# Kernel optimization log

Measured on AMD Instinct MI355X. Metric: run time of the kernel, lower is better.

Reference implementation:

```python
import jax, jax.numpy as jnp
import numpy as np

B, IN, H1, H2, OUT = 65536, 256, 64, 64, 64
T, ET, ES = 2, 4, 4  # tasks, experts-per-task, shared experts


def _mlp(X, W1, b1, W2, b2, W3, b3):
    # X: [B, IN]; W1: [..., IN, H1] with leading expert dims; returns [B, ..., OUT]
    h = jax.nn.relu(jnp.einsum('bi,...ih->b...h', X, W1) + b1)
    h = jax.nn.relu(jnp.einsum('b...h,...hk->b...k', h, W2) + b2)
    return jnp.einsum('b...k,...ko->b...o', h, W3) + b3


def setup_inputs() -> dict:
    key = jax.random.key(0)
    ks = jax.random.split(key, 16)

    def w(k, shape, fan_in):
        return jax.random.normal(k, shape, dtype=jnp.float32) * (1.0 / np.sqrt(fan_in))

    X = jax.random.normal(ks[0], (B, IN), dtype=jnp.float32)
    # task expert MLPs, batched over [T, ET]
    Wt1 = w(ks[1], (T, ET, IN, H1), IN); bt1 = jnp.zeros((T, ET, H1), jnp.float32)
    Wt2 = w(ks[2], (T, ET, H1, H2), H1); bt2 = jnp.zeros((T, ET, H2), jnp.float32)
    Wt3 = w(ks[3], (T, ET, H2, OUT), H2); bt3 = jnp.zeros((T, ET, OUT), jnp.float32)
    # shared expert MLPs, batched over [ES]
    Ws1 = w(ks[4], (ES, IN, H1), IN); bs1 = jnp.zeros((ES, H1), jnp.float32)
    Ws2 = w(ks[5], (ES, H1, H2), H1); bs2 = jnp.zeros((ES, H2), jnp.float32)
    Ws3 = w(ks[6], (ES, H2, OUT), H2); bs3 = jnp.zeros((ES, OUT), jnp.float32)
    # per-task gates: input -> (ET + ES) logits
    Wg = w(ks[7], (T, IN, ET + ES), IN); bg = jnp.zeros((T, ET + ES), jnp.float32)
    return {"X": X, "Wt1": Wt1, "bt1": bt1, "Wt2": Wt2, "bt2": bt2,
            "Wt3": Wt3, "bt3": bt3, "Ws1": Ws1, "bs1": bs1, "Ws2": Ws2,
            "bs2": bs2, "Ws3": Ws3, "bs3": bs3, "Wg": Wg, "bg": bg}


def reference(X, Wt1, bt1, Wt2, bt2, Wt3, bt3,
              Ws1, bs1, Ws2, bs2, Ws3, bs3, Wg, bg):
    # task experts: [B, T, ET, OUT]; shared experts: [B, ES, OUT]
    task_out = _mlp(X, Wt1, bt1, Wt2, bt2, Wt3, bt3)
    share_out = _mlp(X, Ws1, bs1, Ws2, bs2, Ws3, bs3)
    # concat task + shared experts along the expert axis per task -> [B, T, ET+ES, OUT]
    share_b = jnp.broadcast_to(share_out[:, None], (X.shape[0], T, ES, OUT))
    all_experts = jnp.concatenate([task_out, share_b], axis=2)
    # gates: softmax over experts -> [B, T, ET+ES]
    gates = jax.nn.softmax(jnp.einsum('bi,tie->bte', X, Wg) + bg, axis=-1)
    # gated combine (stack+bmm+squeeze in the original) -> [B, T, OUT]
    return jnp.einsum('bte,bteo->bto', gates, all_experts)
```

## Files before the change

### kernel.cpp

```cpp
#include <hip/hip_runtime.h>
#include <hip/hip_fp16.h>


#define B_TOT   65536
#define IN_DIM  256
#define HD      64
#define NE      12
#define U_A2 49152
#define U_A3 61440
#define U_AG 73728
#define FRAG_BYTES (75776*16)

typedef _Float16 half8  __attribute__((ext_vector_type(8)));
typedef float    f32x16 __attribute__((ext_vector_type(16)));
typedef float    f32x4  __attribute__((ext_vector_type(4)));
typedef unsigned u32x4  __attribute__((ext_vector_type(4)));

__device__ __forceinline__ unsigned short f2h(float x){
  return __builtin_bit_cast(unsigned short, (_Float16)x);
}
__device__ __forceinline__ float h2f(unsigned short u){
  return (float)__builtin_bit_cast(_Float16, u);
}
__device__ __forceinline__ void split2(float x, unsigned short& h, unsigned short& l){
  h = f2h(x); l = f2h(x - h2f(h));
}
__device__ __forceinline__ half8 FRG(u32x4 u){ return __builtin_bit_cast(half8, u); }
__device__ __forceinline__ f32x16 MF(half8 a, half8 b, f32x16 c){
  return __builtin_amdgcn_mfma_f32_32x32x16_f16(a, b, c, 0, 0, 0);
}
__device__ __forceinline__ f32x16 Z16(){
  f32x16 z;
#pragma unroll
  for (int i=0;i<16;i++) z[i]=0.f;
  return z;
}
__device__ __forceinline__ u32x4 lds16(const short* base, int row, int kb){
  return *(const u32x4*)((const char*)base + row*512 + (kb ^ ((row&7)<<4)));
}

__global__ __launch_bounds__(256) void prep(
    const float* __restrict__ Wt1, const float* __restrict__ Ws1,
    const float* __restrict__ Wt2, const float* __restrict__ Ws2,
    const float* __restrict__ Wt3, const float* __restrict__ Ws3,
    const float* __restrict__ Wg,  u32x4* __restrict__ fr){
  int id = blockIdx.x*256 + threadIdx.x;
  if (id >= 37888) return;
  int lane = id & 63;
  int kq   = lane >> 5;
  int row  = lane & 31;
  float v[8];
  unsigned ubase;
  if (id < 24576){
    int r = id >> 6; int kt = r & 15; int rt = (r>>4)&1; int e = r>>5;
    const float* W = (e<8) ? (Wt1 + (size_t)e*(IN_DIM*HD))
                           : (Ws1 + (size_t)(e-8)*(IN_DIM*HD));
    int h = rt*32 + row;
#pragma unroll
    for (int j=0;j<8;j++){ int k = kt*16 + kq*8 + j; v[j] = W[k*HD + h]; }
    ubase = (unsigned)(e*4096 + ((rt*16+kt)*2)*64 + lane);
  } else if (id < 30720){
    int r = (id-24576) >> 6; int kt = r & 3; int rt = (r>>2)&1; int e = r>>3;
    const float* W = (e<8) ? (Wt2 + (size_t)e*(HD*HD))
                           : (Ws2 + (size_t)(e-8)*(HD*HD));
    int h = rt*32 + row;
#pragma unroll
    for (int j=0;j<8;j++){ int k = kt*16 + kq*8 + j; v[j] = W[k*HD + h]; }
    ubase = (unsigned)(U_A2 + e*1024 + ((rt*4+kt)*2)*64 + lane);
  } else if (id < 36864){
    int r = (id-30720) >> 6; int kt = r & 3; int rt = (r>>2)&1; int e = r>>3;
    const float* W = (e<8) ? (Wt3 + (size_t)e*(HD*HD))
                           : (Ws3 + (size_t)(e-8)*(HD*HD));
    int h = rt*32 + row;
#pragma unroll
    for (int j=0;j<8;j++){ int k = kt*16 + kq*8 + j; v[j] = W[k*HD + h]; }
    ubase = (unsigned)(U_A3 + e*1024 + ((rt*4+kt)*2)*64 + lane);
  } else {
    int r = (id-36864) >> 6; int kt = r;
    int g = row;
#pragma unroll
    for (int j=0;j<8;j++){
      int k = kt*16 + kq*8 + j;
      v[j] = (g < 16) ? Wg[(size_t)(g>>3)*(IN_DIM*8) + k*8 + (g&7)] : 0.f;
    }
    ubase = (unsigned)(U_AG + (kt*2)*64 + lane);
  }
  u32x4 uh, ul;
#pragma unroll
  for (int p=0;p<4;p++){
    unsigned short h0,l0,h1,l1;
    split2(v[2*p],h0,l0); split2(v[2*p+1],h1,l1);
    uh[p] = (unsigned)h0 | ((unsigned)h1<<16);
    ul[p] = (unsigned)l0 | ((unsigned)l1<<16);
  }
  fr[ubase]     = uh;
  fr[ubase+64]  = ul;
}

__device__ __forceinline__ void epi12(const f32x16& A, const float* bp, int rt, int hi,
                                      unsigned* oh, unsigned* ol){
#pragma unroll
  for (int p=0;p<8;p++){
    const int j0=2*p, j1=2*p+1;
    float v0 = A[j0] + bp[rt*32 + 8*(j0>>2) + 4*hi + (j0&3)];
    float v1 = A[j1] + bp[rt*32 + 8*(j1>>2) + 4*hi + (j1&3)];
    v0 = fmaxf(v0, 0.f); v1 = fmaxf(v1, 0.f);
    unsigned short h0,l0,h1,l1;
    split2(v0,h0,l0); split2(v1,h1,l1);
    oh[p] = (unsigned)h0 | ((unsigned)h1<<16);
    ol[p] = (unsigned)l0 | ((unsigned)l1<<16);
  }
}

__device__ __forceinline__ half8 bfrag(const unsigned* pk, int kl, int hi){
  unsigned p0 = pk[4*kl+0], p1 = pk[4*kl+1], p2 = pk[4*kl+2], p3 = pk[4*kl+3];
  unsigned q0 = (unsigned)__shfl_xor((int)p0, 32, 64);
  unsigned q1 = (unsigned)__shfl_xor((int)p1, 32, 64);
  unsigned q2 = (unsigned)__shfl_xor((int)p2, 32, 64);
  unsigned q3 = (unsigned)__shfl_xor((int)p3, 32, 64);
  u32x4 u;
  u.x = hi ? q2 : p0;
  u.y = hi ? q3 : p1;
  u.z = hi ? p2 : q0;
  u.w = hi ? p3 : q1;
  return FRG(u);
}

__device__ __forceinline__ void epi3(const f32x16& A, const float* bp, int rt, int ct,
                                     int hi, int li, int e, int lrow0, char* obase){
  unsigned f[8];
#pragma unroll
  for (int p=0;p<8;p++){
    const int j0=2*p, j1=2*p+1;
    float v0 = A[j0] + bp[rt*32 + 8*(j0>>2) + 4*hi + (j0&3)];
    float v1 = A[j1] + bp[rt*32 + 8*(j1>>2) + 4*hi + (j1&3)];
    f[p] = (unsigned)f2h(v0) | ((unsigned)f2h(v1)<<16);
  }
  unsigned g[8];
#pragma unroll
  for (int p=0;p<8;p++) g[p] = (unsigned)__shfl_xor((int)f[p], 32, 64);
  char* ob = obase + ((size_t)(lrow0 + ct*32 + li)*NE + e)*128 + rt*64;
#pragma unroll
  for (int q=0;q<4;q++){
    u32x4 w;
    w.x = hi ? g[2*q]   : f[2*q];
    w.y = hi ? g[2*q+1] : f[2*q+1];
    w.z = hi ? f[2*q]   : g[2*q];
    w.w = hi ? f[2*q+1] : g[2*q+1];
    if ((q>>1) == hi) *(u32x4*)(ob + q*16) = w;
  }
}

#define MM3(ACC, AH, AL, BH, BL) do { \
    ACC = MF(AH,BH,ACC); ACC = MF(AH,BL,ACC); ACC = MF(AL,BH,ACC); } while(0)

__global__ __launch_bounds__(256,2) void moe(
    const float* __restrict__ X,
    const float* __restrict__ bt1, const float* __restrict__ bs1,
    const float* __restrict__ bt2, const float* __restrict__ bs2,
    const float* __restrict__ bt3, const float* __restrict__ bs3,
    const float* __restrict__ bg,  const u32x4* __restrict__ fr,
    float* __restrict__ gout, char* __restrict__ oout, int crow0){
  __shared__ __align__(16) short Xh[64*256];
  __shared__ __align__(16) short Xl[64*256];
  const int t = threadIdx.x;
  const int lrow0 = blockIdx.x*64;
  const int grow0 = crow0 + lrow0;

  {
    const int r = t>>2, cq = t&3;
    const float* xp = X + (size_t)(grow0 + r)*IN_DIM + cq*64;
#pragma unroll
    for (int gq=0; gq<8; gq++){
      f32x4 v0 = *(const f32x4*)(xp + gq*8);
      f32x4 v1 = *(const f32x4*)(xp + gq*8 + 4);
      float vv[8] = {v0.x,v0.y,v0.z,v0.w, v1.x,v1.y,v1.z,v1.w};
      u32x4 uh, ul;
#pragma unroll
      for (int p=0;p<4;p++){
        unsigned short h0,l0,h1,l1;
        split2(vv[2*p],h0,l0); split2(vv[2*p+1],h1,l1);
        uh[p] = (unsigned)h0 | ((unsigned)h1<<16);
        ul[p] = (unsigned)l0 | ((unsigned)l1<<16);
      }
      int kb = (cq*64 + gq*8)*2;
      int addr = r*512 + (kb ^ ((r&7)<<4));
      *(u32x4*)((char*)Xh + addr) = uh;
      *(u32x4*)((char*)Xl + addr) = ul;
    }
  }
  __syncthreads();

  const int wave = t>>6, lane = t&63, li = lane&31, hi = lane>>5;

  if (wave == 0){
    f32x16 g0 = Z16(), g1 = Z16();
    const u32x4* AG = fr + U_AG + lane;
#pragma unroll
    for (int kt=0; kt<16; ++kt){
      half8 ah = FRG(AG[(kt*2+0)*64]);
      half8 al = FRG(AG[(kt*2+1)*64]);
      int kb = kt*32 + hi*16;
      half8 xh0 = FRG(lds16(Xh, li,    kb)), xl0 = FRG(lds16(Xl, li,    kb));
      half8 xh1 = FRG(lds16(Xh, li+32, kb)), xl1 = FRG(lds16(Xl, li+32, kb));
      MM3(g0, ah, al, xh0, xl0);
      MM3(g1, ah, al, xh1, xl1);
    }
#pragma unroll
    for (int ct=0; ct<2; ++ct){
      const f32x16& G = ct ? g1 : g0;
      float own[8], par[8];
#pragma unroll
      for (int j=0;j<8;j++) own[j] = G[j] + bg[8*(j>>2) + 4*hi + (j&3)];
#pragma unroll
      for (int j=0;j<8;j++) par[j] = __shfl_xor(own[j], 32, 64);
      float m0 = fmaxf(fmaxf(fmaxf(own[0],own[1]),fmaxf(own[2],own[3])),
                       fmaxf(fmaxf(par[0],par[1]),fmaxf(par[2],par[3])));
      float m1 = fmaxf(fmaxf(fmaxf(own[4],own[5]),fmaxf(own[6],own[7])),
                       fmaxf(fmaxf(par[4],par[5]),fmaxf(par[6],par[7])));
      float eo[8], ep[8];
#pragma unroll
      for (int j=0;j<4;j++){ eo[j]   = __expf(own[j]-m0);   ep[j]   = __expf(par[j]-m0); }
#pragma unroll
      for (int j=4;j<8;j++){ eo[j]   = __expf(own[j]-m1);   ep[j]   = __expf(par[j]-m1); }
      float s0 = eo[0]+eo[1]+eo[2]+eo[3]+ep[0]+ep[1]+ep[2]+ep[3];
      float s1 = eo[4]+eo[5]+eo[6]+eo[7]+ep[4]+ep[5]+ep[6]+ep[7];
      float i0 = 1.f/s0, i1 = 1.f/s1;
      if (hi == 0){
        float* gp = gout + (size_t)(lrow0 + ct*32 + li)*16;
        f32x4 w;
        w.x=eo[0]*i0; w.y=eo[1]*i0; w.z=eo[2]*i0; w.w=eo[3]*i0; ((f32x4*)gp)[0]=w;
        w.x=ep[0]*i0; w.y=ep[1]*i0; w.z=ep[2]*i0; w.w=ep[3]*i0; ((f32x4*)gp)[1]=w;
        w.x=eo[4]*i1; w.y=eo[5]*i1; w.z=eo[6]*i1; w.w=eo[7]*i1; ((f32x4*)gp)[2]=w;
        w.x=ep[4]*i1; w.y=ep[5]*i1; w.z=ep[6]*i1; w.w=ep[7]*i1; ((f32x4*)gp)[3]=w;
      }
    }
  }

  unsigned opkh[2][2][8], opkl[2][2][8];
#pragma unroll 1
  for (int ei=0; ei<3; ++ei){
    const int e = wave*3 + ei;
    f32x16 a00=Z16(), a01=Z16(), a10=Z16(), a11=Z16();
    const u32x4* A1 = fr + e*4096 + lane;
#pragma unroll
    for (int kt=0; kt<16; ++kt){
      half8 ah0 = FRG(A1[( kt     *2+0)*64]);
      half8 al0 = FRG(A1[( kt     *2+1)*64]);
      half8 ah1 = FRG(A1[((16+kt) *2+0)*64]);
      half8 al1 = FRG(A1[((16+kt) *2+1)*64]);
      int kb = kt*32 + hi*16;
      half8 xh0 = FRG(lds16(Xh, li,    kb)), xl0 = FRG(lds16(Xl, li,    kb));
      half8 xh1 = FRG(lds16(Xh, li+32, kb)), xl1 = FRG(lds16(Xl, li+32, kb));
      MM3(a00, ah0, al0, xh0, xl0);
      MM3(a01, ah0, al0, xh1, xl1);
      MM3(a10, ah1, al1, xh0, xl0);
      MM3(a11, ah1, al1, xh1, xl1);
    }
    const float* b1 = (e<8)? bt1+e*64 : bs1+(e-8)*64;
    epi12(a00,b1,0,hi,opkh[0][0],opkl[0][0]);
    epi12(a01,b1,0,hi,opkh[0][1],opkl[0][1]);
    epi12(a10,b1,1,hi,opkh[1][0],opkl[1][0]);
    epi12(a11,b1,1,hi,opkh[1][1],opkl[1][1]);
    f32x16 c00=Z16(), c01=Z16(), c10=Z16(), c11=Z16();
    const u32x4* A2 = fr + U_A2 + e*1024 + lane;
#pragma unroll
    for (int kt=0; kt<4; ++kt){
      half8 ah0 = FRG(A2[( kt    *2+0)*64]);
      half8 al0 = FRG(A2[( kt    *2+1)*64]);
      half8 ah1 = FRG(A2[((4+kt) *2+0)*64]);
      half8 al1 = FRG(A2[((4+kt) *2+1)*64]);
      const int rs = kt>>1, kl = kt&1;
      half8 bh0 = bfrag(opkh[rs][0], kl, hi), bl0 = bfrag(opkl[rs][0], kl, hi);
      half8 bh1 = bfrag(opkh[rs][1], kl, hi), bl1 = bfrag(opkl[rs][1], kl, hi);
      MM3(c00, ah0, al0, bh0, bl0);
      MM3(c01, ah0, al0, bh1, bl1);
      MM3(c10, ah1, al1, bh0, bl0);
      MM3(c11, ah1, al1, bh1, bl1);
    }
    const float* b2 = (e<8)? bt2+e*64 : bs2+(e-8)*64;
    epi12(c00,b2,0,hi,opkh[0][0],opkl[0][0]);
    epi12(c01,b2,0,hi,opkh[0][1],opkl[0][1]);
    epi12(c10,b2,1,hi,opkh[1][0],opkl[1][0]);
    epi12(c11,b2,1,hi,opkh[1][1],opkl[1][1]);
    f32x16 d00=Z16(), d01=Z16(), d10=Z16(), d11=Z16();
    const u32x4* A3 = fr + U_A3 + e*1024 + lane;
#pragma unroll
    for (int kt=0; kt<4; ++kt){
      half8 ah0 = FRG(A3[( kt    *2+0)*64]);
      half8 al0 = FRG(A3[( kt    *2+1)*64]);
      half8 ah1 = FRG(A3[((4+kt) *2+0)*64]);
      half8 al1 = FRG(A3[((4+kt) *2+1)*64]);
      const int rs = kt>>1, kl = kt&1;
      half8 bh0 = bfrag(opkh[rs][0], kl, hi), bl0 = bfrag(opkl[rs][0], kl, hi);
      half8 bh1 = bfrag(opkh[rs][1], kl, hi), bl1 = bfrag(opkl[rs][1], kl, hi);
      MM3(d00, ah0, al0, bh0, bl0);
      MM3(d01, ah0, al0, bh1, bl1);
      MM3(d10, ah1, al1, bh0, bl0);
      MM3(d11, ah1, al1, bh1, bl1);
    }
    const float* b3 = (e<8)? bt3+e*64 : bs3+(e-8)*64;
    epi3(d00,b3,0,0,hi,li,e,lrow0,oout);
    epi3(d01,b3,0,1,hi,li,e,lrow0,oout);
    epi3(d10,b3,1,0,hi,li,e,lrow0,oout);
    epi3(d11,b3,1,1,hi,li,e,lrow0,oout);
  }
}

__device__ __forceinline__ float2 uph(unsigned u){
  __half2 h = __builtin_bit_cast(__half2, u);
  return __half22float2(h);
}
__global__ __launch_bounds__(256) void comb(
    const u32x4* __restrict__ o, const float* __restrict__ g,
    float* __restrict__ out, int rows, int crow0){
  int tid = blockIdx.x*256 + threadIdx.x;
  if (tid >= rows*4) return;
  int bl = tid>>2, quad = tid&3;
  const u32x4* ob = o + (size_t)bl*96 + quad*2;
  const f32x4* gp = (const f32x4*)(g + (size_t)bl*16);
  f32x4 G0=gp[0], G1=gp[1], G2=gp[2], G3=gp[3];
  float gt[16] = {G0.x,G0.y,G0.z,G0.w, G1.x,G1.y,G1.z,G1.w,
                  G2.x,G2.y,G2.z,G2.w, G3.x,G3.y,G3.z,G3.w};
  float s0[16], s1[16];
#pragma unroll
  for (int i=0;i<16;i++){ s0[i]=0.f; s1[i]=0.f; }
#pragma unroll
  for (int e=0;e<12;e++){
    u32x4 u0 = ob[e*8], u1 = ob[e*8+1];
    float w0 = (e<4) ? gt[e]   : ((e>=8) ? gt[e-4] : 0.f);
    float w1 = (e>=4 && e<8) ? gt[e+4] : ((e>=8) ? gt[e+4] : 0.f);
    float v[16];
#pragma unroll
    for (int p=0;p<4;p++){
      float2 f0 = uph(u0[p]); v[2*p]   = f0.x; v[2*p+1]   = f0.y;
      float2 f1 = uph(u1[p]); v[8+2*p] = f1.x; v[8+2*p+1] = f1.y;
    }
#pragma unroll
    for (int i=0;i<16;i++){ s0[i] += w0*v[i]; s1[i] += w1*v[i]; }
  }
  size_t b = (size_t)crow0 + bl;
  float* op = out + b*128 + quad*16;
#pragma unroll
  for (int p=0;p<4;p++){
    f32x4 w; w.x=s0[4*p]; w.y=s0[4*p+1]; w.z=s0[4*p+2]; w.w=s0[4*p+3];
    *(f32x4*)(op + 4*p) = w;
  }
#pragma unroll
  for (int p=0;p<4;p++){
    f32x4 w; w.x=s1[4*p]; w.y=s1[4*p+1]; w.z=s1[4*p+2]; w.w=s1[4*p+3];
    *(f32x4*)(op + 64 + 4*p) = w;
  }
}

extern "C" void kernel_launch(void* const* d_in, const int* in_sizes, int n_in,
                              void* d_out, int out_size, void* d_ws, size_t ws_size,
                              hipStream_t stream){
  const float* X   = (const float*)d_in[0];
  const float* Wt1 = (const float*)d_in[1];
  const float* bt1 = (const float*)d_in[2];
  const float* Wt2 = (const float*)d_in[3];
  const float* bt2 = (const float*)d_in[4];
  const float* Wt3 = (const float*)d_in[5];
  const float* bt3 = (const float*)d_in[6];
  const float* Ws1 = (const float*)d_in[7];
  const float* bs1 = (const float*)d_in[8];
  const float* Ws2 = (const float*)d_in[9];
  const float* bs2 = (const float*)d_in[10];
  const float* Ws3 = (const float*)d_in[11];
  const float* bs3 = (const float*)d_in[12];
  const float* Wg  = (const float*)d_in[13];
  const float* bg  = (const float*)d_in[14];

  char*  ws = (char*)d_ws;
  u32x4* fr = (u32x4*)ws;
  size_t avail = ws_size > (size_t)FRAG_BYTES ? ws_size - FRAG_BYTES : 0;
  int chunk = B_TOT;
  while (chunk > 64 && (size_t)chunk*1600 > avail) chunk >>= 1;

  hipLaunchKernelGGL(prep, dim3(148), dim3(256), 0, stream,
                     Wt1, Ws1, Wt2, Ws2, Wt3, Ws3, Wg, fr);
  for (int r0 = 0; r0 < B_TOT; r0 += chunk){
    float* gts = (float*)(ws + FRAG_BYTES);
    char*  ob  = ws + FRAG_BYTES + (size_t)chunk*64;
    hipLaunchKernelGGL(moe, dim3(chunk/64), dim3(256), 0, stream,
                       X, bt1, bs1, bt2, bs2, bt3, bs3, bg, fr, gts, ob, r0);
    hipLaunchKernelGGL(comb, dim3((chunk*4+255)/256), dim3(256), 0, stream,
                       (const u32x4*)ob, gts, (float*)d_out, chunk, r0);
  }
}
```

Before: 381.8 us.

## Split MoE kernel into per-expert single-wave blocks with pre-split X in global

X is now converted to fp16 hi/lo pairs once by a separate xsplit kernel that writes to global memory, replacing the per-block LDS staging. The fused moe kernel becomes moe1, which runs one 64-thread wave per (expert, row-group) pair, with an extra block type for the gate softmax. This is meant to raise parallelism and occupancy and to drop the LDS footprint and the block-wide barrier. Layers 2 and 3 are now processed per column tile to lower register pressure, and the expert-output scratch layout is changed to expert-major, with comb re-indexed to match. The cost is extra global traffic for the split X, since every expert block re-reads the hi/lo data from global or L2.

```diff
diff --git a/kernel.cpp b/kernel.cpp
--- a/kernel.cpp
+++ b/kernel.cpp
@@ -15,6 +15,7 @@
 typedef float    f32x16 __attribute__((ext_vector_type(16)));
 typedef float    f32x4  __attribute__((ext_vector_type(4)));
 typedef unsigned u32x4  __attribute__((ext_vector_type(4)));
+typedef unsigned u32x2  __attribute__((ext_vector_type(2)));
 
 __device__ __forceinline__ unsigned short f2h(float x){
   return __builtin_bit_cast(unsigned short, (_Float16)x);
@@ -34,9 +35,6 @@
 #pragma unroll
   for (int i=0;i<16;i++) z[i]=0.f;
   return z;
-}
-__device__ __forceinline__ u32x4 lds16(const short* base, int row, int kb){
-  return *(const u32x4*)((const char*)base + row*512 + (kb ^ ((row&7)<<4)));
 }
 
 __global__ __launch_bounds__(256) void prep(
@@ -97,6 +95,25 @@
   fr[ubase+64]  = ul;
 }
 
+__global__ __launch_bounds__(256) void xsplit(
+    const float* __restrict__ X, u32x2* __restrict__ xh,
+    u32x2* __restrict__ xl, int n4){
+  int tid = blockIdx.x*256 + threadIdx.x;
+  if (tid >= n4) return;
+  f32x4 v = ((const f32x4*)X)[tid];
+  float vv[4] = {v.x, v.y, v.z, v.w};
+  u32x2 uh, ul;
+#pragma unroll
+  for (int p=0;p<2;p++){
+    unsigned short h0,l0,h1,l1;
+    split2(vv[2*p],h0,l0); split2(vv[2*p+1],h1,l1);
+    uh[p] = (unsigned)h0 | ((unsigned)h1<<16);
+    ul[p] = (unsigned)l0 | ((unsigned)l1<<16);
+  }
+  xh[tid] = uh;
+  xl[tid] = ul;
+}
+
 __device__ __forceinline__ void epi12(const f32x16& A, const float* bp, int rt, int hi,
                                       unsigned* oh, unsigned* ol){
 #pragma unroll
@@ -127,7 +144,7 @@
 }
 
 __device__ __forceinline__ void epi3(const f32x16& A, const float* bp, int rt, int ct,
-                                     int hi, int li, int e, int lrow0, char* obase){
+                                     int hi, int li, size_t ebase, char* osc){
   unsigned f[8];
 #pragma unroll
   for (int p=0;p<8;p++){
@@ -139,7 +156,7 @@
   unsigned g[8];
 #pragma unroll
   for (int p=0;p<8;p++) g[p] = (unsigned)__shfl_xor((int)f[p], 32, 64);
-  char* ob = obase + ((size_t)(lrow0 + ct*32 + li)*NE + e)*128 + rt*64;
+  char* ob = osc + (ebase + (size_t)(ct*32 + li))*128 + rt*64;
 #pragma unroll
   for (int q=0;q<4;q++){
     u32x4 w;
@@ -154,64 +171,42 @@
 #define MM3(ACC, AH, AL, BH, BL) do { \
     ACC = MF(AH,BH,ACC); ACC = MF(AH,BL,ACC); ACC = MF(AL,BH,ACC); } while(0)
 
-__global__ __launch_bounds__(256,2) void moe(
-    const float* __restrict__ X,
+__global__ __launch_bounds__(64,3) void moe1(
+    const char* __restrict__ xh, const char* __restrict__ xl,
     const float* __restrict__ bt1, const float* __restrict__ bs1,
     const float* __restrict__ bt2, const float* __restrict__ bs2,
     const float* __restrict__ bt3, const float* __restrict__ bs3,
     const float* __restrict__ bg,  const u32x4* __restrict__ fr,
-    float* __restrict__ gout, char* __restrict__ oout, int crow0){
-  __shared__ __align__(16) short Xh[64*256];
-  __shared__ __align__(16) short Xl[64*256];
-  const int t = threadIdx.x;
-  const int lrow0 = blockIdx.x*64;
-  const int grow0 = crow0 + lrow0;
-
-  {
-    const int r = t>>2, cq = t&3;
-    const float* xp = X + (size_t)(grow0 + r)*IN_DIM + cq*64;
-#pragma unroll
-    for (int gq=0; gq<8; gq++){
-      f32x4 v0 = *(const f32x4*)(xp + gq*8);
-      f32x4 v1 = *(const f32x4*)(xp + gq*8 + 4);
-      float vv[8] = {v0.x,v0.y,v0.z,v0.w, v1.x,v1.y,v1.z,v1.w};
-      u32x4 uh, ul;
-#pragma unroll
-      for (int p=0;p<4;p++){
-        unsigned short h0,l0,h1,l1;
-        split2(vv[2*p],h0,l0); split2(vv[2*p+1],h1,l1);
-        uh[p] = (unsigned)h0 | ((unsigned)h1<<16);
-        ul[p] = (unsigned)l0 | ((unsigned)l1<<16);
-      }
-      int kb = (cq*64 + gq*8)*2;
-      int addr = r*512 + (kb ^ ((r&7)<<4));
-      *(u32x4*)((char*)Xh + addr) = uh;
-      *(u32x4*)((char*)Xl + addr) = ul;
-    }
-  }
-  __syncthreads();
-
-  const int wave = t>>6, lane = t&63, li = lane&31, hi = lane>>5;
-
-  if (wave == 0){
+    float* __restrict__ gout, char* __restrict__ osc, int G, int Crows){
+  const int e = blockIdx.x / G;
+  const int g = blockIdx.x - e*G;
+  const int lane = threadIdx.x, li = lane&31, hi = lane>>5;
+
+  const char* xh0p = xh + (size_t)(g*64 +      li)*512 + hi*16;
+  const char* xh1p = xh + (size_t)(g*64 + 32 + li)*512 + hi*16;
+  const char* xl0p = xl + (size_t)(g*64 +      li)*512 + hi*16;
+  const char* xl1p = xl + (size_t)(g*64 + 32 + li)*512 + hi*16;
+
+  if (e == 12){
     f32x16 g0 = Z16(), g1 = Z16();
     const u32x4* AG = fr + U_AG + lane;
 #pragma unroll
     for (int kt=0; kt<16; ++kt){
       half8 ah = FRG(AG[(kt*2+0)*64]);
       half8 al = FRG(AG[(kt*2+1)*64]);
-      int kb = kt*32 + hi*16;
-      half8 xh0 = FRG(lds16(Xh, li,    kb)), xl0 = FRG(lds16(Xl, li,    kb));
-      half8 xh1 = FRG(lds16(Xh, li+32, kb)), xl1 = FRG(lds16(Xl, li+32, kb));
-      MM3(g0, ah, al, xh0, xl0);
-      MM3(g1, ah, al, xh1, xl1);
+      half8 xh0 = FRG(*(const u32x4*)(xh0p + kt*32));
+      half8 xl0v= FRG(*(const u32x4*)(xl0p + kt*32));
+      half8 xh1 = FRG(*(const u32x4*)(xh1p + kt*32));
+      half8 xl1v= FRG(*(const u32x4*)(xl1p + kt*32));
+      MM3(g0, ah, al, xh0, xl0v);
+      MM3(g1, ah, al, xh1, xl1v);
     }
 #pragma unroll
     for (int ct=0; ct<2; ++ct){
-      const f32x16& G = ct ? g1 : g0;
+      const f32x16& Gc = ct ? g1 : g0;
       float own[8], par[8];
 #pragma unroll
-      for (int j=0;j<8;j++) own[j] = G[j] + bg[8*(j>>2) + 4*hi + (j&3)];
+      for (int j=0;j<8;j++) own[j] = Gc[j] + bg[8*(j>>2) + 4*hi + (j&3)];
 #pragma unroll
       for (int j=0;j<8;j++) par[j] = __shfl_xor(own[j], 32, 64);
       float m0 = fmaxf(fmaxf(fmaxf(own[0],own[1]),fmaxf(own[2],own[3])),
@@ -220,14 +215,14 @@
                        fmaxf(fmaxf(par[4],par[5]),fmaxf(par[6],par[7])));
       float eo[8], ep[8];
 #pragma unroll
-      for (int j=0;j<4;j++){ eo[j]   = __expf(own[j]-m0);   ep[j]   = __expf(par[j]-m0); }
-#pragma unroll
-      for (int j=4;j<8;j++){ eo[j]   = __expf(own[j]-m1);   ep[j]   = __expf(par[j]-m1); }
+      for (int j=0;j<4;j++){ eo[j] = __expf(own[j]-m0); ep[j] = __expf(par[j]-m0); }
+#pragma unroll
+      for (int j=4;j<8;j++){ eo[j] = __expf(own[j]-m1); ep[j] = __expf(par[j]-m1); }
       float s0 = eo[0]+eo[1]+eo[2]+eo[3]+ep[0]+ep[1]+ep[2]+ep[3];
       float s1 = eo[4]+eo[5]+eo[6]+eo[7]+ep[4]+ep[5]+ep[6]+ep[7];
       float i0 = 1.f/s0, i1 = 1.f/s1;
       if (hi == 0){
-        float* gp = gout + (size_t)(lrow0 + ct*32 + li)*16;
+        float* gp = gout + (size_t)(g*64 + ct*32 + li)*16;
         f32x4 w;
         w.x=eo[0]*i0; w.y=eo[1]*i0; w.z=eo[2]*i0; w.w=eo[3]*i0; ((f32x4*)gp)[0]=w;
         w.x=ep[0]*i0; w.y=ep[1]*i0; w.z=ep[2]*i0; w.w=ep[3]*i0; ((f32x4*)gp)[1]=w;
@@ -235,12 +230,11 @@
         w.x=ep[4]*i1; w.y=ep[5]*i1; w.z=ep[6]*i1; w.w=ep[7]*i1; ((f32x4*)gp)[3]=w;
       }
     }
-  }
-
-  unsigned opkh[2][2][8], opkl[2][2][8];
-#pragma unroll 1
-  for (int ei=0; ei<3; ++ei){
-    const int e = wave*3 + ei;
+    return;
+  }
+
+  unsigned o1h[2][2][8], o1l[2][2][8];
+  {
     f32x16 a00=Z16(), a01=Z16(), a10=Z16(), a11=Z16();
     const u32x4* A1 = fr + e*4096 + lane;
 #pragma unroll
@@ -249,61 +243,62 @@
       half8 al0 = FRG(A1[( kt     *2+1)*64]);
       half8 ah1 = FRG(A1[((16+kt) *2+0)*64]);
       half8 al1 = FRG(A1[((16+kt) *2+1)*64]);
-      int kb = kt*32 + hi*16;
-      half8 xh0 = FRG(lds16(Xh, li,    kb)), xl0 = FRG(lds16(Xl, li,    kb));
-      half8 xh1 = FRG(lds16(Xh, li+32, kb)), xl1 = FRG(lds16(Xl, li+32, kb));
-      MM3(a00, ah0, al0, xh0, xl0);
-      MM3(a01, ah0, al0, xh1, xl1);
-      MM3(a10, ah1, al1, xh0, xl0);
-      MM3(a11, ah1, al1, xh1, xl1);
+      half8 xh0 = FRG(*(const u32x4*)(xh0p + kt*32));
+      half8 xl0v= FRG(*(const u32x4*)(xl0p + kt*32));
+      half8 xh1 = FRG(*(const u32x4*)(xh1p + kt*32));
+      half8 xl1v= FRG(*(const u32x4*)(xl1p + kt*32));
+      MM3(a00, ah0, al0, xh0, xl0v);
+      MM3(a01, ah0, al0, xh1, xl1v);
+      MM3(a10, ah1, al1, xh0, xl0v);
+      MM3(a11, ah1, al1, xh1, xl1v);
     }
     const float* b1 = (e<8)? bt1+e*64 : bs1+(e-8)*64;
-    epi12(a00,b1,0,hi,opkh[0][0],opkl[0][0]);
-    epi12(a01,b1,0,hi,opkh[0][1],opkl[0][1]);
-    epi12(a10,b1,1,hi,opkh[1][0],opkl[1][0]);
-    epi12(a11,b1,1,hi,opkh[1][1],opkl[1][1]);
-    f32x16 c00=Z16(), c01=Z16(), c10=Z16(), c11=Z16();
-    const u32x4* A2 = fr + U_A2 + e*1024 + lane;
-#pragma unroll
-    for (int kt=0; kt<4; ++kt){
-      half8 ah0 = FRG(A2[( kt    *2+0)*64]);
-      half8 al0 = FRG(A2[( kt    *2+1)*64]);
-      half8 ah1 = FRG(A2[((4+kt) *2+0)*64]);
-      half8 al1 = FRG(A2[((4+kt) *2+1)*64]);
-      const int rs = kt>>1, kl = kt&1;
-      half8 bh0 = bfrag(opkh[rs][0], kl, hi), bl0 = bfrag(opkl[rs][0], kl, hi);
-      half8 bh1 = bfrag(opkh[rs][1], kl, hi), bl1 = bfrag(opkl[rs][1], kl, hi);
-      MM3(c00, ah0, al0, bh0, bl0);
-      MM3(c01, ah0, al0, bh1, bl1);
-      MM3(c10, ah1, al1, bh0, bl0);
-      MM3(c11, ah1, al1, bh1, bl1);
-    }
-    const float* b2 = (e<8)? bt2+e*64 : bs2+(e-8)*64;
-    epi12(c00,b2,0,hi,opkh[0][0],opkl[0][0]);
-    epi12(c01,b2,0,hi,opkh[0][1],opkl[0][1]);
-    epi12(c10,b2,1,hi,opkh[1][0],opkl[1][0]);
-    epi12(c11,b2,1,hi,opkh[1][1],opkl[1][1]);
-    f32x16 d00=Z16(), d01=Z16(), d10=Z16(), d11=Z16();
-    const u32x4* A3 = fr + U_A3 + e*1024 + lane;
-#pragma unroll
-    for (int kt=0; kt<4; ++kt){
-      half8 ah0 = FRG(A3[( kt    *2+0)*64]);
-      half8 al0 = FRG(A3[( kt    *2+1)*64]);
-      half8 ah1 = FRG(A3[((4+kt) *2+0)*64]);
-      half8 al1 = FRG(A3[((4+kt) *2+1)*64]);
-      const int rs = kt>>1, kl = kt&1;
-      half8 bh0 = bfrag(opkh[rs][0], kl, hi), bl0 = bfrag(opkl[rs][0], kl, hi);
-      half8 bh1 = bfrag(opkh[rs][1], kl, hi), bl1 = bfrag(opkl[rs][1], kl, hi);
-      MM3(d00, ah0, al0, bh0, bl0);
-      MM3(d01, ah0, al0, bh1, bl1);
-      MM3(d10, ah1, al1, bh0, bl0);
-      MM3(d11, ah1, al1, bh1, bl1);
-    }
-    const float* b3 = (e<8)? bt3+e*64 : bs3+(e-8)*64;
-    epi3(d00,b3,0,0,hi,li,e,lrow0,oout);
-    epi3(d01,b3,0,1,hi,li,e,lrow0,oout);
-    epi3(d10,b3,1,0,hi,li,e,lrow0,oout);
-    epi3(d11,b3,1,1,hi,li,e,lrow0,oout);
+    epi12(a00,b1,0,hi,o1h[0][0],o1l[0][0]);
+    epi12(a01,b1,0,hi,o1h[0][1],o1l[0][1]);
+    epi12(a10,b1,1,hi,o1h[1][0],o1l[1][0]);
+    epi12(a11,b1,1,hi,o1h[1][1],o1l[1][1]);
+  }
+  const float* b2 = (e<8)? bt2+e*64 : bs2+(e-8)*64;
+  const float* b3 = (e<8)? bt3+e*64 : bs3+(e-8)*64;
+  const size_t ebase = (size_t)e*Crows + (size_t)g*64;
+
+#pragma unroll
+  for (int ct=0; ct<2; ++ct){
+    unsigned o2h[2][8], o2l[2][8];
+    {
+      f32x16 c0=Z16(), c1=Z16();
+      const u32x4* A2 = fr + U_A2 + e*1024 + lane;
+#pragma unroll
+      for (int kt=0; kt<4; ++kt){
+        half8 ah0 = FRG(A2[( kt    *2+0)*64]);
+        half8 al0 = FRG(A2[( kt    *2+1)*64]);
+        half8 ah1 = FRG(A2[((4+kt) *2+0)*64]);
+        half8 al1 = FRG(A2[((4+kt) *2+1)*64]);
+        const int rs = kt>>1, kl = kt&1;
+        half8 bh = bfrag(o1h[rs][ct], kl, hi), bl = bfrag(o1l[rs][ct], kl, hi);
+        MM3(c0, ah0, al0, bh, bl);
+        MM3(c1, ah1, al1, bh, bl);
+      }
+      epi12(c0,b2,0,hi,o2h[0],o2l[0]);
+      epi12(c1,b2,1,hi,o2h[1],o2l[1]);
+    }
+    {
+      f32x16 d0=Z16(), d1=Z16();
+      const u32x4* A3 = fr + U_A3 + e*1024 + lane;
+#pragma unroll
+      for (int kt=0; kt<4; ++kt){
+        half8 ah0 = FRG(A3[( kt    *2+0)*64]);
+        half8 al0 = FRG(A3[( kt    *2+1)*64]);
+        half8 ah1 = FRG(A3[((4+kt) *2+0)*64]);
+        half8 al1 = FRG(A3[((4+kt) *2+1)*64]);
+        const int rs = kt>>1, kl = kt&1;
+        half8 bh = bfrag(o2h[rs], kl, hi), bl = bfrag(o2l[rs], kl, hi);
+        MM3(d0, ah0, al0, bh, bl);
+        MM3(d1, ah1, al1, bh, bl);
+      }
+      epi3(d0,b3,0,ct,hi,li,ebase,osc);
+      epi3(d1,b3,1,ct,hi,li,ebase,osc);
+    }
   }
 }
 
@@ -312,45 +307,28 @@
   return __half22float2(h);
 }
 __global__ __launch_bounds__(256) void comb(
-    const u32x4* __restrict__ o, const float* __restrict__ g,
-    float* __restrict__ out, int rows, int crow0){
+    const char* __restrict__ osc, const float* __restrict__ g,
+    float* __restrict__ out, int Crows, int crow0){
   int tid = blockIdx.x*256 + threadIdx.x;
-  if (tid >= rows*4) return;
-  int bl = tid>>2, quad = tid&3;
-  const u32x4* ob = o + (size_t)bl*96 + quad*2;
-  const f32x4* gp = (const f32x4*)(g + (size_t)bl*16);
-  f32x4 G0=gp[0], G1=gp[1], G2=gp[2], G3=gp[3];
-  float gt[16] = {G0.x,G0.y,G0.z,G0.w, G1.x,G1.y,G1.z,G1.w,
-                  G2.x,G2.y,G2.z,G2.w, G3.x,G3.y,G3.z,G3.w};
-  float s0[16], s1[16];
-#pragma unroll
-  for (int i=0;i<16;i++){ s0[i]=0.f; s1[i]=0.f; }
+  if (tid >= Crows*16) return;
+  int b = tid>>4, o4 = tid&15;
+  const float* gp = g + (size_t)b*16;
+  float s0[4] = {0.f,0.f,0.f,0.f}, s1[4] = {0.f,0.f,0.f,0.f};
 #pragma unroll
   for (int e=0;e<12;e++){
-    u32x4 u0 = ob[e*8], u1 = ob[e*8+1];
-    float w0 = (e<4) ? gt[e]   : ((e>=8) ? gt[e-4] : 0.f);
-    float w1 = (e>=4 && e<8) ? gt[e+4] : ((e>=8) ? gt[e+4] : 0.f);
-    float v[16];
-#pragma unroll
-    for (int p=0;p<4;p++){
-      float2 f0 = uph(u0[p]); v[2*p]   = f0.x; v[2*p+1]   = f0.y;
-      float2 f1 = uph(u1[p]); v[8+2*p] = f1.x; v[8+2*p+1] = f1.y;
-    }
-#pragma unroll
-    for (int i=0;i<16;i++){ s0[i] += w0*v[i]; s1[i] += w1*v[i]; }
-  }
-  size_t b = (size_t)crow0 + bl;
-  float* op = out + b*128 + quad*16;
-#pragma unroll
-  for (int p=0;p<4;p++){
-    f32x4 w; w.x=s0[4*p]; w.y=s0[4*p+1]; w.z=s0[4*p+2]; w.w=s0[4*p+3];
-    *(f32x4*)(op + 4*p) = w;
-  }
-#pragma unroll
-  for (int p=0;p<4;p++){
-    f32x4 w; w.x=s1[4*p]; w.y=s1[4*p+1]; w.z=s1[4*p+2]; w.w=s1[4*p+3];
-    *(f32x4*)(op + 64 + 4*p) = w;
-  }
+    const u32x2 u = *(const u32x2*)(osc + ((size_t)e*Crows + b)*128 + o4*8);
+    float2 f0 = uph(u.x), f1 = uph(u.y);
+    float v[4] = {f0.x, f0.y, f1.x, f1.y};
+    float w0 = (e<4) ? gp[e] : (e>=8 ? gp[e-4] : 0.f);
+    float w1 = (e<4) ? 0.f  : (e<8 ? gp[4+e] : gp[e+4]);
+#pragma unroll
+    for (int i=0;i<4;i++){ s0[i] += w0*v[i]; s1[i] += w1*v[i]; }
+  }
+  float* op = out + ((size_t)(crow0+b))*128 + o4*4;
+  f32x4 w0v; w0v.x=s0[0]; w0v.y=s0[1]; w0v.z=s0[2]; w0v.w=s0[3];
+  f32x4 w1v; w1v.x=s1[0]; w1v.y=s1[1]; w1v.z=s1[2]; w1v.w=s1[3];
+  *(f32x4*)op        = w0v;
+  *(f32x4*)(op + 64) = w1v;
 }
 
 extern "C" void kernel_launch(void* const* d_in, const int* in_sizes, int n_in,
@@ -372,20 +350,26 @@
   const float* Wg  = (const float*)d_in[13];
   const float* bg  = (const float*)d_in[14];
 
-  char*  ws = (char*)d_ws;
+  char* ws = (char*)d_ws;
   u32x4* fr = (u32x4*)ws;
-  size_t avail = ws_size > (size_t)FRAG_BYTES ? ws_size - FRAG_BYTES : 0;
-  int chunk = B_TOT;
-  while (chunk > 64 && (size_t)chunk*1600 > avail) chunk >>= 1;
+
+  int C = B_TOT;
+  while (C > 64 && (size_t)FRAG_BYTES + (size_t)C*2624 > ws_size) C >>= 1;
+  char* xh  = ws + FRAG_BYTES;
+  char* xl  = xh + (size_t)C*512;
+  char* osc = xl + (size_t)C*512;
+  float* gts = (float*)(osc + (size_t)C*1536);
+  const int G = C/64;
 
   hipLaunchKernelGGL(prep, dim3(148), dim3(256), 0, stream,
                      Wt1, Ws1, Wt2, Ws2, Wt3, Ws3, Wg, fr);
-  for (int r0 = 0; r0 < B_TOT; r0 += chunk){
-    float* gts = (float*)(ws + FRAG_BYTES);
-    char*  ob  = ws + FRAG_BYTES + (size_t)chunk*64;
-    hipLaunchKernelGGL(moe, dim3(chunk/64), dim3(256), 0, stream,
-                       X, bt1, bs1, bt2, bs2, bt3, bs3, bg, fr, gts, ob, r0);
-    hipLaunchKernelGGL(comb, dim3((chunk*4+255)/256), dim3(256), 0, stream,
-                       (const u32x4*)ob, gts, (float*)d_out, chunk, r0);
-  }
-}
+  for (int r0 = 0; r0 < B_TOT; r0 += C){
+    hipLaunchKernelGGL(xsplit, dim3(C/4), dim3(256), 0, stream,
+                       X + (size_t)r0*IN_DIM, (u32x2*)xh, (u32x2*)xl, C*64);
+    hipLaunchKernelGGL(moe1, dim3(13*G), dim3(64), 0, stream,
+                       xh, xl, bt1, bs1, bt2, bs2, bt3, bs3, bg, fr,
+                       gts, osc, G, C);
+    hipLaunchKernelGGL(comb, dim3(C/16), dim3(256), 0, stream,
+                       osc, gts, (float*)d_out, C, r0);
+  }
+}
```

Result: slower. 410.2 us (+7.5%).
